# Kernel optimization log

Measured on AMD Instinct MI355X. Metric: run time of the kernel, lower is better.

The kernel has to match this reference:

```python
import jax, jax.numpy as jnp
import numpy as np
from jax.scipy.special import logsumexp

# config constants (match init_kwargs)
EPS_SH, IT_SH = 0.05, 10      # shared-space sinkhorn
EPS_AN, IT_AN = 0.05, 10      # anchor-space sinkhorn
TEMP_SAIL, BIAS_SAIL = 10.0, 0.0
CLAMP = 1e-8


def _rownorm(x):
    return x / jnp.clip(jnp.linalg.norm(x, axis=1, keepdims=True), CLAMP)


def cosine_similarity_matrix(a, b):
    return _rownorm(a) @ _rownorm(b).T


def sinkhorn(dist, epsilon, max_iter):
    """Log-domain Sinkhorn with uniform marginals. dist: (nx, ny)."""
    nx, ny = dist.shape
    M = -dist / epsilon                      # (nx, ny) log kernel
    log_a = -jnp.log(jnp.float32(nx))
    log_b = -jnp.log(jnp.float32(ny))

    def step(carry, _):
        u, v = carry
        u = log_a - logsumexp(M + v[None, :], axis=1)
        v = log_b - logsumexp(M + u[:, None], axis=0)
        return (u, v), None

    init = (jnp.zeros((nx,), M.dtype), jnp.zeros((ny,), M.dtype))
    (u, v), _ = jax.lax.scan(step, init, None, length=max_iter)
    log_plan = M + u[:, None] + v[None, :]
    return jnp.exp(log_plan), log_plan


def setup_inputs() -> dict:
    key = jax.random.key(0)
    ks = jax.random.split(key, 8)
    return {
        "fX_pairs": jax.random.normal(ks[0], (2048, 256), jnp.float32),
        "fY_pairs": jax.random.normal(ks[1], (2048, 256), jnp.float32),
        "X":        jax.random.normal(ks[2], (4096, 768), jnp.float32),
        "Y":        jax.random.normal(ks[3], (4096, 512), jnp.float32),
        "fX":       jax.random.normal(ks[4], (4096, 256), jnp.float32),
        "fY":       jax.random.normal(ks[5], (4096, 256), jnp.float32),
        "X_anchor": jax.random.normal(ks[6], (4096, 768), jnp.float32),
        "Y_anchor": jax.random.normal(ks[7], (4096, 512), jnp.float32),
    }


def _forward(fX_pairs, fY_pairs, X, Y, fX, fY, X_anchor, Y_anchor):
    # --- anchor covariances ---
    Xa, Ya = _rownorm(X_anchor), _rownorm(Y_anchor)
    Na = jnp.float32(Xa.shape[0])
    Sxx = (Xa.T @ Xa) / Na
    Syy = (Ya.T @ Ya) / Na
    Sxy = (Xa.T @ Ya) / Na

    # --- latent-space transport plans (shared sinkhorn) ---
    plan_p, logp_p = sinkhorn(-cosine_similarity_matrix(fX_pairs, fY_pairs), EPS_SH, IT_SH)
    plan_u, logp_u = sinkhorn(-cosine_similarity_matrix(fX, fY), EPS_SH, IT_SH)

    # --- marginal loss: marginals should be uniform ---
    def marginal_loss(plan):
        nx, ny = plan.shape
        a = jnp.full((nx,), 1.0 / nx, plan.dtype)
        b = jnp.full((ny,), 1.0 / ny, plan.dtype)
        return ((plan.sum(1) - a) ** 2).sum() + ((plan.sum(0) - b) ** 2).sum()

    L_marg = marginal_loss(plan_p) + marginal_loss(plan_u)

    # --- SAIL sigmoid contrastive loss on pairs ---
    N = fX_pairs.shape[0]
    cos = cosine_similarity_matrix(fX_pairs, fY_pairs)
    target = -1.0 + 2.0 * jnp.eye(N, dtype=cos.dtype)
    L_sail = -jnp.mean(jax.nn.log_sigmoid(cos * TEMP_SAIL * target - BIAS_SAIL))

    # --- supervised explicit: cosine distance on pairs ---
    L_exp = jnp.mean((1.0 - (_rownorm(fX_pairs) * _rownorm(fY_pairs)).sum(-1)) / 2.0)

    # --- supervised implicit: diag of log plan vs uniform identity ---
    L_imp = -jnp.mean(jnp.diag(logp_p) + jnp.log(jnp.float32(N)))

    # --- anchor-space plan (torch.no_grad -> stop_gradient) ---
    nX = jnp.clip(jnp.sqrt((X * (X @ Sxx)).sum(-1, keepdims=True)), CLAMP)
    nY = jnp.clip(jnp.sqrt((Y * (Y @ Syy)).sum(-1, keepdims=True)), CLAMP)
    Xn, Yn = X / nX, Y / nY
    plan_a, logp_a = jax.lax.stop_gradient(sinkhorn(-(Xn @ Sxy @ Yn.T), EPS_AN, IT_AN))
    Xn = jax.lax.stop_gradient(Xn)
    Yn = jax.lax.stop_gradient(Yn)

    # --- semisupervised OT: KL(plan_anchor || plan_latent) ---
    L_ot = (plan_a * (logp_a - logp_u)).sum()

    # --- semisupervised divergence (frobenius) ---
    fXn, fYn = _rownorm(fX), _rownorm(fY)
    norm1 = (((Xn.T @ Xn) @ Sxy @ (Yn.T @ Yn)) * Sxy).sum()
    norm2 = ((fXn.T @ fXn) * (fYn.T @ fYn)).sum()
    dot = (((Xn.T @ fXn) @ (fYn.T @ Yn)) * Sxy).sum()
    cste = jnp.float32(X.shape[0] * Y.shape[0])
    L_div = (norm1 + norm2 - 2.0 * dot) / cste

    # --- unsupervised Gromov-Wasserstein-style loss ---
    Xu = jax.lax.stop_gradient(_rownorm(X))
    Yu = jax.lax.stop_gradient(_rownorm(Y))
    Kx = Xu @ Xu.T   # (Nx, Nx)
    Ky = Yu @ Yu.T   # (Ny, Ny)
    a = plan_u.sum(1)
    b = plan_u.sum(0)
    L_gw = (a @ (Kx ** 2) @ a + b @ (Ky ** 2) @ b
            - 2.0 * ((Kx @ plan_u @ Ky) * plan_u).sum())

    return L_marg + L_sail + L_exp + L_imp + L_ot + L_div + L_gw


def reference(fX_pairs, fY_pairs, X, Y, fX, fY, X_anchor, Y_anchor):
    return _forward(fX_pairs, fY_pairs, X, Y, fX, fY, X_anchor, Y_anchor)
```

## Files before the change

kernel.cpp:

```cpp
#include <hip/hip_runtime.h>
#include <hip/hip_bf16.h>
#include <math.h>

using u16 = unsigned short;
using s8v = __attribute__((ext_vector_type(8))) short;
using s4v = __attribute__((ext_vector_type(4))) short;
using f4v = __attribute__((ext_vector_type(4))) float;

__device__ __forceinline__ float b2f(u16 x) {
    unsigned int u = ((unsigned int)x) << 16;
    return __uint_as_float(u);
}
__device__ __forceinline__ u16 f2b(float f) {
    unsigned int x = __float_as_uint(f);
    unsigned int r = x + 0x7fffu + ((x >> 16) & 1u);
    return (u16)(r >> 16);
}

__device__ __forceinline__ void a16(u16* lds, const u16* g) {
    __builtin_amdgcn_global_load_lds((__attribute__((address_space(1))) void*)g,
                                     (__attribute__((address_space(3))) void*)lds,
                                     16, 0, 0);
}

__device__ __forceinline__ float block_sum(float v, float* buf) {
    int t = threadIdx.x;
    buf[t] = v; __syncthreads();
    for (int s = 128; s > 0; s >>= 1) {
        if (t < s) buf[t] += buf[t + s];
        __syncthreads();
    }
    float r = buf[0];
    __syncthreads();
    return r;
}

__device__ __forceinline__ float wave_sum(float v) {
#pragma unroll
    for (int off = 32; off; off >>= 1) v += __shfl_xor(v, off, 64);
    return v;
}

__device__ __forceinline__ void block_atomic4(float wval, float* slot) {
    __shared__ float wb[4];
    int lane = threadIdx.x & 63, wv = threadIdx.x >> 6;
    if (lane == 0) wb[wv] = wval;
    __syncthreads();
    if (threadIdx.x == 0) atomicAdd(slot, wb[0] + wb[1] + wb[2] + wb[3]);
}

#define TBM 128
#define TBN 128
#define TBK 32

template<int EPI>
__global__ __launch_bounds__(256)
void gemm_bt(const u16* __restrict__ A, const u16* __restrict__ B,
             float* __restrict__ Cf, u16* __restrict__ Cb,
             int M, int N, int K, int ld, float alpha)
{
    __shared__ __align__(16) u16 As[TBM * TBK];
    __shared__ __align__(16) u16 Bs[TBN * TBK];

    const int tid  = threadIdx.x;
    const int lane = tid & 63;
    const int wave = tid >> 6;
    const int wm   = (wave >> 1) * 64;
    const int wn   = (wave & 1) * 64;
    const int l16  = lane & 15;
    const int q4   = lane >> 4;
    const size_t row0 = (size_t)blockIdx.y * TBM;
    const size_t col0 = (size_t)blockIdx.x * TBN;
    const int kOff = blockIdx.z * K;

    f4v acc[4][4];
#pragma unroll
    for (int mt = 0; mt < 4; ++mt)
#pragma unroll
        for (int nt = 0; nt < 4; ++nt)
#pragma unroll
            for (int r = 0; r < 4; ++r)
                acc[mt][nt][r] = 0.f;

    const int ar0 = wave * 32 + (lane >> 2);
    const int ar1 = ar0 + 16;
    const int akk = (lane & 3) * 8;
    const u16* gA0 = A + (row0 + ar0) * ld + kOff + akk;
    const u16* gA1 = A + (row0 + ar1) * ld + kOff + akk;
    const u16* gB0 = B + (col0 + ar0) * ld + kOff + akk;
    const u16* gB1 = B + (col0 + ar1) * ld + kOff + akk;
    u16* lA0 = As + wave * 1024;
    u16* lA1 = As + wave * 1024 + 512;
    u16* lB0 = Bs + wave * 1024;
    u16* lB1 = Bs + wave * 1024 + 512;

    for (int k0 = 0; k0 < K; k0 += TBK) {
        __syncthreads();
        a16(lA0, gA0 + k0);
        a16(lA1, gA1 + k0);
        a16(lB0, gB0 + k0);
        a16(lB1, gB1 + k0);
        __syncthreads();

        s8v af[4], bfr[4];
#pragma unroll
        for (int mt = 0; mt < 4; ++mt)
            af[mt] = *(const s8v*)(As + (wm + mt * 16 + l16) * TBK + q4 * 8);
#pragma unroll
        for (int nt = 0; nt < 4; ++nt)
            bfr[nt] = *(const s8v*)(Bs + (wn + nt * 16 + l16) * TBK + q4 * 8);
#pragma unroll
        for (int mt = 0; mt < 4; ++mt)
#pragma unroll
            for (int nt = 0; nt < 4; ++nt)
                acc[mt][nt] = __builtin_amdgcn_mfma_f32_16x16x32_bf16(af[mt], bfr[nt], acc[mt][nt], 0, 0, 0);
    }

#pragma unroll
    for (int mt = 0; mt < 4; ++mt)
#pragma unroll
        for (int nt = 0; nt < 4; ++nt)
#pragma unroll
            for (int r = 0; r < 4; ++r) {
                size_t row = row0 + wm + mt * 16 + q4 * 4 + r;
                size_t col = col0 + wn + nt * 16 + l16;
                float v = acc[mt][nt][r] * alpha;
                if (EPI == 0)      Cf[row * (size_t)N + col] = v;
                else if (EPI == 1) Cb[row * (size_t)N + col] = f2b(v);
                else               atomicAdd(&Cf[row * (size_t)N + col], v);
            }
}

struct BG { const u16* A; const u16* B; float* C; int M, Nn, tN, tEnd; };
struct BGArgs { BG d[6]; int n; float alpha; };

__global__ __launch_bounds__(256)
void bgemm(BGArgs g)
{
    __shared__ __align__(16) u16 As[TBM * TBK];
    __shared__ __align__(16) u16 Bs[TBN * TBK];

    int bi = 0;
    while (bi < g.n - 1 && (int)blockIdx.x >= g.d[bi].tEnd) ++bi;
    const BG& d = g.d[bi];
    const int tStart = bi ? g.d[bi - 1].tEnd : 0;
    const int local = blockIdx.x - tStart;
    const int tm = local / d.tN;
    const int tn = local - tm * d.tN;

    const int tid  = threadIdx.x;
    const int lane = tid & 63;
    const int wave = tid >> 6;
    const int wm   = (wave >> 1) * 64;
    const int wn   = (wave & 1) * 64;
    const int l16  = lane & 15;
    const int q4   = lane >> 4;
    const size_t row0 = (size_t)tm * TBM;
    const size_t col0 = (size_t)tn * TBN;
    const int kOff = blockIdx.y * 512;
    const int ld = 4096;

    f4v acc[4][4];
#pragma unroll
    for (int mt = 0; mt < 4; ++mt)
#pragma unroll
        for (int nt = 0; nt < 4; ++nt)
#pragma unroll
            for (int r = 0; r < 4; ++r)
                acc[mt][nt][r] = 0.f;

    const int ar0 = wave * 32 + (lane >> 2);
    const int ar1 = ar0 + 16;
    const int akk = (lane & 3) * 8;
    const u16* gA0 = d.A + (row0 + ar0) * ld + kOff + akk;
    const u16* gA1 = d.A + (row0 + ar1) * ld + kOff + akk;
    const u16* gB0 = d.B + (col0 + ar0) * ld + kOff + akk;
    const u16* gB1 = d.B + (col0 + ar1) * ld + kOff + akk;
    u16* lA0 = As + wave * 1024;
    u16* lA1 = As + wave * 1024 + 512;
    u16* lB0 = Bs + wave * 1024;
    u16* lB1 = Bs + wave * 1024 + 512;

    for (int k0 = 0; k0 < 512; k0 += TBK) {
        __syncthreads();
        a16(lA0, gA0 + k0);
        a16(lA1, gA1 + k0);
        a16(lB0, gB0 + k0);
        a16(lB1, gB1 + k0);
        __syncthreads();

        s8v af[4], bfr[4];
#pragma unroll
        for (int mt = 0; mt < 4; ++mt)
            af[mt] = *(const s8v*)(As + (wm + mt * 16 + l16) * TBK + q4 * 8);
#pragma unroll
        for (int nt = 0; nt < 4; ++nt)
            bfr[nt] = *(const s8v*)(Bs + (wn + nt * 16 + l16) * TBK + q4 * 8);
#pragma unroll
        for (int mt = 0; mt < 4; ++mt)
#pragma unroll
            for (int nt = 0; nt < 4; ++nt)
                acc[mt][nt] = __builtin_amdgcn_mfma_f32_16x16x32_bf16(af[mt], bfr[nt], acc[mt][nt], 0, 0, 0);
    }

#pragma unroll
    for (int mt = 0; mt < 4; ++mt)
#pragma unroll
        for (int nt = 0; nt < 4; ++nt)
#pragma unroll
            for (int r = 0; r < 4; ++r) {
                size_t row = row0 + wm + mt * 16 + q4 * 4 + r;
                size_t col = col0 + wn + nt * 16 + l16;
                atomicAdd(&d.C[row * (size_t)d.Nn + col], acc[mt][nt][r] * g.alpha);
            }
}

struct RN { const float* in; u16* out; int C; int rEnd; };
struct RNArgs { RN d[8]; int n; };

__global__ __launch_bounds__(256)
void rownorm_batch(RNArgs a) {
    int gw = (blockIdx.x * 256 + threadIdx.x) >> 6;
    int lane = threadIdx.x & 63;
    int i = 0;
    while (i < a.n - 1 && gw >= a.d[i].rEnd) ++i;
    if (gw >= a.d[i].rEnd) return;
    int row = gw - (i ? a.d[i - 1].rEnd : 0);
    int C = a.d[i].C;
    const float4* r4 = (const float4*)(a.d[i].in + (size_t)row * C);
    int nv = C >> 2;
    float ss = 0.f;
    for (int c = lane; c < nv; c += 64) {
        float4 v = r4[c];
        ss += v.x * v.x + v.y * v.y + v.z * v.z + v.w * v.w;
    }
    ss = wave_sum(ss);
    float inv = 1.f / fmaxf(sqrtf(ss), 1e-8f);
    s4v* o4 = (s4v*)(a.d[i].out + (size_t)row * C);
    for (int c = lane; c < nv; c += 64) {
        float4 v = r4[c];
        s4v o;
        o[0] = (short)f2b(v.x * inv); o[1] = (short)f2b(v.y * inv);
        o[2] = (short)f2b(v.z * inv); o[3] = (short)f2b(v.w * inv);
        o4[c] = o;
    }
}

__global__ __launch_bounds__(256)
void mahal_w(const u16* __restrict__ Xh, const float* __restrict__ XS,
             u16* __restrict__ out, int nrows, int C) {
    int row = (blockIdx.x * 256 + threadIdx.x) >> 6;
    int lane = threadIdx.x & 63;
    if (row >= nrows) return;
    const s4v* x4 = (const s4v*)(Xh + (size_t)row * C);
    const float4* s4 = (const float4*)(XS + (size_t)row * C);
    int nv = C >> 2;
    float s = 0.f;
    for (int c = lane; c < nv; c += 64) {
        s4v x = x4[c]; float4 v = s4[c];
        s += b2f((u16)x[0]) * v.x + b2f((u16)x[1]) * v.y
           + b2f((u16)x[2]) * v.z + b2f((u16)x[3]) * v.w;
    }
    s = wave_sum(s);
    float inv = 1.f / fmaxf(sqrtf(fmaxf(s, 0.f)), 1e-8f);
    s4v* o4 = (s4v*)(out + (size_t)row * C);
    for (int c = lane; c < nv; c += 64) {
        s4v x = x4[c], o;
#pragma unroll
        for (int k = 0; k < 4; ++k) o[k] = (short)f2b(b2f((u16)x[k]) * inv);
        o4[c] = o;
    }
}

struct TP { const u16* in; u16* out; int R, C, tC, tEnd; const float* s; };
struct TPArgs { TP d[6]; int n; };

__global__ __launch_bounds__(256)
void transpose_batch(TPArgs a) {
    __shared__ u16 tile[32][33];
    int t = blockIdx.x;
    int i = 0;
    while (i < a.n - 1 && t >= a.d[i].tEnd) ++i;
    int local = t - (i ? a.d[i - 1].tEnd : 0);
    const TP& d = a.d[i];
    int ty = local / d.tC, tx = local - ty * d.tC;
    int bx = tx * 32, by = ty * 32;
    int lx = threadIdx.x & 31;
    int lyy = threadIdx.x >> 5;
    for (int r = lyy; r < 32; r += 8)
        tile[r][lx] = d.in[(size_t)(by + r) * d.C + bx + lx];
    __syncthreads();
    for (int r = lyy; r < 32; r += 8) {
        u16 val = tile[lx][r];
        if (d.s) val = f2b(b2f(val) * d.s[by + lx]);
        d.out[(size_t)(bx + r) * d.R + by + lx] = val;
    }
}

__global__ __launch_bounds__(256)
void cast_f2b(const float* __restrict__ in, u16* __restrict__ out, int n) {
    for (int i = blockIdx.x * 256 + threadIdx.x; i < n; i += gridDim.x * 256)
        out[i] = f2b(in[i]);
}

__device__ __forceinline__ float row_sumexp(const u16* __restrict__ rowp,
                                            const float* __restrict__ vin,
                                            int ny, float scale, int lane) {
    const s8v* r8 = (const s8v*)rowp;
    const float4* v4 = (const float4*)vin;
    int nv = ny >> 3;
    float s = 0.f;
    for (int c = lane; c < nv; c += 64) {
        s8v v8 = r8[c];
        float4 va = v4[c * 2], vb = v4[c * 2 + 1];
        s += __expf(b2f((u16)v8[0]) * scale + va.x);
        s += __expf(b2f((u16)v8[1]) * scale + va.y);
        s += __expf(b2f((u16)v8[2]) * scale + va.z);
        s += __expf(b2f((u16)v8[3]) * scale + va.w);
        s += __expf(b2f((u16)v8[4]) * scale + vb.x);
        s += __expf(b2f((u16)v8[5]) * scale + vb.y);
        s += __expf(b2f((u16)v8[6]) * scale + vb.z);
        s += __expf(b2f((u16)v8[7]) * scale + vb.w);
    }
    return wave_sum(s);
}

__global__ __launch_bounds__(256)
void row_lse_tri(const u16* __restrict__ C1, const float* __restrict__ v1, float* __restrict__ u1,
                 const u16* __restrict__ C2, const float* __restrict__ v2, float* __restrict__ u2,
                 const u16* __restrict__ C3, const float* __restrict__ v3, float* __restrict__ u3,
                 float scale, float lm12, float lm3) {
    int gw = (blockIdx.x * 256 + threadIdx.x) >> 6;
    int lane = threadIdx.x & 63;
    if (gw < 4096) {
        float s = row_sumexp(C1 + (size_t)gw * 4096, v1, 4096, scale, lane);
        if (lane == 0) u1[gw] = lm12 - __logf(s);
    } else if (gw < 8192) {
        int row = gw - 4096;
        float s = row_sumexp(C2 + (size_t)row * 4096, v2, 4096, scale, lane);
        if (lane == 0) u2[row] = lm12 - __logf(s);
    } else {
        int row = gw - 8192;
        if (row >= 2048) return;
        float s = row_sumexp(C3 + (size_t)row * 2048, v3, 2048, scale, lane);
        if (lane == 0) u3[row] = lm3 - __logf(s);
    }
}

__device__ __forceinline__ float plan_body(const u16* __restrict__ rowp, u16* __restrict__ prow,
                                           float ui, const float* __restrict__ vin,
                                           int ny, float scale, int lane) {
    const s8v* r8 = (const s8v*)rowp;
    s8v* p8 = (s8v*)prow;
    const float4* v4 = (const float4*)vin;
    int nv = ny >> 3;
    float s = 0.f;
    for (int c = lane; c < nv; c += 64) {
        s8v v8 = r8[c], pb;
        float4 va = v4[c * 2], vb = v4[c * 2 + 1];
        float vv[8] = {va.x, va.y, va.z, va.w, vb.x, vb.y, vb.z, vb.w};
#pragma unroll
        for (int k = 0; k < 8; ++k) {
            float p = __expf(b2f((u16)v8[k]) * scale + ui + vv[k]);
            s += p;
            pb[k] = (short)f2b(p);
        }
        if (p8) p8[c] = pb;
    }
    return wave_sum(s);
}

__global__ __launch_bounds__(256)
void plan_quad(const u16* __restrict__ Cu, const u16* __restrict__ CuT,
               const u16* __restrict__ cosp, const u16* __restrict__ cospT,
               const float* __restrict__ uu, const float* __restrict__ vu,
               const float* __restrict__ up, const float* __restrict__ vp,
               u16* __restrict__ plan,
               float* __restrict__ au, float* __restrict__ bu,
               float* __restrict__ ap, float* __restrict__ bp, float scale) {
    int gw = (blockIdx.x * 256 + threadIdx.x) >> 6;
    int lane = threadIdx.x & 63;
    if (gw < 4096) {
        float s = plan_body(Cu + (size_t)gw * 4096, plan + (size_t)gw * 4096, uu[gw], vu, 4096, scale, lane);
        if (lane == 0) au[gw] = s;
    } else if (gw < 8192) {
        int r = gw - 4096;
        float s = plan_body(CuT + (size_t)r * 4096, nullptr, vu[r], uu, 4096, scale, lane);
        if (lane == 0) bu[r] = s;
    } else if (gw < 10240) {
        int r = gw - 8192;
        float s = plan_body(cosp + (size_t)r * 2048, nullptr, up[r], vp, 2048, scale, lane);
        if (lane == 0) ap[r] = s;
    } else {
        int r = gw - 10240;
        if (r >= 2048) return;
        float s = plan_body(cospT + (size_t)r * 2048, nullptr, vp[r], up, 2048, scale, lane);
        if (lane == 0) bp[r] = s;
    }
}

__global__ __launch_bounds__(256)
void marg4(const float* __restrict__ ap, const float* __restrict__ bp,
           const float* __restrict__ au, const float* __restrict__ bu,
           float* __restrict__ slot) {
    const float* sv; int n; float target;
    if (blockIdx.x == 0)      { sv = ap; n = 2048; target = 1.f / 2048.f; }
    else if (blockIdx.x == 1) { sv = bp; n = 2048; target = 1.f / 2048.f; }
    else if (blockIdx.x == 2) { sv = au; n = 4096; target = 1.f / 4096.f; }
    else                      { sv = bu; n = 4096; target = 1.f / 4096.f; }
    int t = threadIdx.x;
    float s = 0.f;
    for (int i = t; i < n; i += 256) { float d = sv[i] - target; s += d * d; }
    __shared__ float buf[256];
    float tot = block_sum(s, buf);
    if (t == 0) atomicAdd(slot, tot);
}

__global__ __launch_bounds__(256)
void ot_row_w(const u16* __restrict__ Ca, const u16* __restrict__ Cu,
              const float* __restrict__ ua, const float* __restrict__ va,
              const float* __restrict__ uu, const float* __restrict__ vu,
              int nrows, int ny, float scale, float* __restrict__ slot) {
    int row = (blockIdx.x * 256 + threadIdx.x) >> 6;
    int lane = threadIdx.x & 63;
    float local = 0.f;
    if (row < nrows) {
        const s8v* ra = (const s8v*)(Ca + (size_t)row * ny);
        const s8v* ru = (const s8v*)(Cu + (size_t)row * ny);
        const float4* va4 = (const float4*)va;
        const float4* vu4 = (const float4*)vu;
        float uai = ua[row], uui = uu[row];
        int nv = ny >> 3;
        for (int c = lane; c < nv; c += 64) {
            s8v a8 = ra[c], u8 = ru[c];
            float4 a0 = va4[c * 2], a1 = va4[c * 2 + 1];
            float4 u0 = vu4[c * 2], u1 = vu4[c * 2 + 1];
            float av[8] = {a0.x, a0.y, a0.z, a0.w, a1.x, a1.y, a1.z, a1.w};
            float uv[8] = {u0.x, u0.y, u0.z, u0.w, u1.x, u1.y, u1.z, u1.w};
#pragma unroll
            for (int k = 0; k < 8; ++k) {
                float lpa = b2f((u16)a8[k]) * scale + uai + av[k];
                float lpu = b2f((u16)u8[k]) * scale + uui + uv[k];
                local += __expf(lpa) * (lpa - lpu);
            }
        }
    }
    local = wave_sum(local);
    block_atomic4(local, slot);
}

__global__ __launch_bounds__(256)
void sail_row_w(const u16* __restrict__ cosb, int n, float temp, float* __restrict__ slot) {
    int row = (blockIdx.x * 256 + threadIdx.x) >> 6;
    int lane = threadIdx.x & 63;
    float local = 0.f;
    if (row < n) {
        const s8v* r8 = (const s8v*)(cosb + (size_t)row * n);
        int nv = n >> 3;
        for (int c = lane; c < nv; c += 64) {
            s8v v8 = r8[c];
#pragma unroll
            for (int k = 0; k < 8; ++k) {
                int j = c * 8 + k;
                float cv = b2f((u16)v8[k]);
                float wgt = cv * ((j == row) ? temp : -temp);
                local -= fminf(wgt, 0.f) - log1pf(__expf(-fabsf(wgt)));
            }
        }
    }
    local = wave_sum(local);
    block_atomic4(local, slot);
}

__global__ __launch_bounds__(256)
void diag2(const u16* __restrict__ cosb, const float* __restrict__ up,
           const float* __restrict__ vp, int n, float scale,
           float* __restrict__ slotExp, float* __restrict__ slotImp) {
    int t = threadIdx.x;
    float e = 0.f, im = 0.f;
    float logn = logf((float)n);
    for (int i = t; i < n; i += 256) {
        float c = b2f(cosb[(size_t)i * n + i]);
        e  += (1.f - c) * 0.5f;
        im += scale * c + up[i] + vp[i] + logn;
    }
    __shared__ float buf[256];
    float te = block_sum(e, buf);
    float ti = block_sum(im, buf);
    if (t == 0) { atomicAdd(slotExp, te); atomicAdd(slotImp, ti); }
}

__global__ __launch_bounds__(256)
void dotT(const float* __restrict__ Mf, const u16* __restrict__ Tb, int R, int Cc,
          float* __restrict__ slot) {
    int t = threadIdx.x;
    int total = R * Cc;
    float local = 0.f;
    for (int idx = blockIdx.x * 256 + t; idx < total; idx += gridDim.x * 256) {
        int a = idx / Cc, b = idx - a * Cc;
        local += Mf[idx] * b2f(Tb[(size_t)b * R + a]);
    }
    __shared__ float buf[256];
    float tot = block_sum(local, buf);
    if (t == 0) atomicAdd(slot, tot);
}

__global__ __launch_bounds__(256)
void dot_bb(const u16* __restrict__ A, const u16* __restrict__ B, int n,
            float* __restrict__ slot) {
    int t = threadIdx.x;
    float local = 0.f;
    for (int i = blockIdx.x * 256 + t; i < n; i += gridDim.x * 256)
        local += b2f(A[i]) * b2f(B[i]);
    __shared__ float buf[256];
    float tot = block_sum(local, buf);
    if (t == 0) atomicAdd(slot, tot);
}

__global__ __launch_bounds__(256)
void dot3(const float* __restrict__ A, const float* __restrict__ B, const float* __restrict__ C,
          int na, int nb, int nc, float* __restrict__ sA, float* __restrict__ sB, float* __restrict__ sC) {
    const float* p; int n, b0, nblk; float* slot;
    if (blockIdx.x < 32)      { p = A; n = na; b0 = 0;  nblk = 32; slot = sA; }
    else if (blockIdx.x < 48) { p = B; n = nb; b0 = 32; nblk = 16; slot = sB; }
    else                      { p = C; n = nc; b0 = 48; nblk = 16; slot = sC; }
    int t = threadIdx.x;
    float local = 0.f;
    for (int i = (blockIdx.x - b0) * 256 + t; i < n; i += nblk * 256) {
        float v = p[i]; local += v * v;
    }
    __shared__ float buf[256];
    float tot = block_sum(local, buf);
    if (t == 0) atomicAdd(slot, tot);
}

__global__ void combine(const float* __restrict__ s, float* __restrict__ out) {
    if (threadIdx.x == 0 && blockIdx.x == 0) {
        float Np = 2048.f;
        float Nu2 = 4096.f * 4096.f;
        float total = s[0]
                    + s[1] / (Np * Np)
                    + s[2] / Np
                    - s[3] / Np
                    + s[4]
                    + (s[5] + s[6] - 2.f * s[7]) / Nu2
                    + s[8] + s[9] - 2.f * s[10];
        out[0] = total;
    }
}

extern "C" void kernel_launch(void* const* d_in, const int* in_sizes, int n_in,
                              void* d_out, int out_size, void* d_ws, size_t ws_size,
                              hipStream_t stream) {
    const float* fXp_in = (const float*)d_in[0];
    const float* fYp_in = (const float*)d_in[1];
    const float* X_in   = (const float*)d_in[2];
    const float* Y_in   = (const float*)d_in[3];
    const float* fX_in  = (const float*)d_in[4];
    const float* fY_in  = (const float*)d_in[5];
    const float* Xa_in  = (const float*)d_in[6];
    const float* Ya_in  = (const float*)d_in[7];
    float* out = (float*)d_out;

    char* w = (char*)d_ws;
    size_t off = 0;
    auto alloc = [&](size_t bytes) -> char* {
        char* p = w + off;
        off += (bytes + 255) & ~(size_t)255;
        return p;
    };

    const size_t N = 4096, Np = 2048, DX = 768, DY = 512, DF = 256;

    const size_t SLOT = N * N * 2;
    char* S1 = alloc(SLOT);
    char* S2 = alloc(SLOT);
    char* S3 = alloc(SLOT);
    char* S4 = alloc(SLOT);
    char* S5 = alloc(SLOT);

    u16* Xa   = (u16*)S1;
    u16* Cu   = (u16*)S1;
    u16* T1T  = (u16*)S1;
    u16* Ya   = (u16*)S2;
    u16* CuT  = (u16*)S2;
    u16* XuT  = (u16*)S2;
    u16* YuT  = (u16*)(S2 + N * DX * 2);
    u16* Ca   = (u16*)S3;
    u16* XsT  = (u16*)S3;
    u16* YsT  = (u16*)(S3 + N * DX * 2);
    u16* XaT  = (u16*)S4;
    u16* YaT  = (u16*)(S4 + N * DX * 2);
    float* XS = (float*)S4;
    u16* XnT  = (u16*)S4;
    u16* YnT  = (u16*)(S4 + N * DX * 2);
    u16* CaT  = (u16*)S4;
    float* YS = (float*)S5;
    u16* Tb   = (u16*)S5;
    u16* plan = (u16*)S5;

    u16* fXp  = (u16*)alloc(Np * DF * 2);
    u16* fYp  = (u16*)alloc(Np * DF * 2);
    u16* fXn  = (u16*)alloc(N * DF * 2);
    u16* fYn  = (u16*)alloc(N * DF * 2);
    u16* fXnT = (u16*)alloc(N * DF * 2);
    u16* fYnT = (u16*)alloc(N * DF * 2);
    u16* Xu   = (u16*)alloc(N * DX * 2);
    u16* Yu   = (u16*)alloc(N * DY * 2);
    u16* Xn   = (u16*)alloc(N * DX * 2);
    u16* Yn   = (u16*)alloc(N * DY * 2);
    u16* Sxx  = (u16*)alloc(DX * DX * 2);
    u16* Syy  = (u16*)alloc(DY * DY * 2);
    u16* SxyT = (u16*)alloc(DY * DX * 2);
    u16* Gx   = (u16*)alloc(DX * DX * 2);
    u16* Gy   = (u16*)alloc(DY * DY * 2);
    u16* Gfx  = (u16*)alloc(DF * DF * 2);
    u16* Gfy  = (u16*)alloc(DF * DF * 2);
    u16* A1b  = (u16*)alloc(DX * DF * 2);
    u16* B1Tb = (u16*)alloc(DY * DF * 2);
    u16* Hb   = (u16*)alloc(DX * DY * 2);
    u16* cosp = (u16*)alloc(Np * Np * 2);
    u16* cospT= (u16*)alloc(Np * Np * 2);
    float* ap = (float*)alloc(Np * 4);
    float* bp = (float*)alloc(Np * 4);
    float* au = (float*)alloc(N * 4);
    float* bu = (float*)alloc(N * 4);

    char* zero_begin = w + off;
    float* slots = (float*)alloc(64 * 4);
    float* up = (float*)alloc(Np * 4);
    float* vp = (float*)alloc(Np * 4);
    float* uu = (float*)alloc(N * 4);
    float* vu = (float*)alloc(N * 4);
    float* ua = (float*)alloc(N * 4);
    float* va = (float*)alloc(N * 4);
    float* SxxF  = (float*)alloc(DX * DX * 4);
    float* SyyF  = (float*)alloc(DY * DY * 4);
    float* SxyTF = (float*)alloc(DY * DX * 4);
    float* GxF   = (float*)alloc(DX * DX * 4);
    float* GyF   = (float*)alloc(DY * DY * 4);
    float* GfxF  = (float*)alloc(DF * DF * 4);
    float* GfyF  = (float*)alloc(DF * DF * 4);
    float* A1F   = (float*)alloc(DX * DF * 4);
    float* B1F   = (float*)alloc(DY * DF * 4);
    float* HbF   = (float*)alloc(DX * DY * 4);
    float* H2    = (float*)alloc(DX * DY * 4);
    float* D1    = (float*)alloc(DX * DY * 4);
    float* W1F   = (float*)alloc(DX * DX * 4);
    float* W2F   = (float*)alloc(DY * DY * 4);
    float* MF    = (float*)alloc(DX * DY * 4);
    size_t zero_bytes = (size_t)((w + off) - zero_begin);

    const float SCALE = 20.f;

#define GEMM_F32(A_, B_, C_, M_, N_, K_, al_) \
    gemm_bt<0><<<dim3((N_) / 128, (M_) / 128), 256, 0, stream>>>((A_), (B_), (C_), nullptr, (M_), (N_), (K_), (K_), (al_))
#define GEMM_B16(A_, B_, C_, M_, N_, K_, al_) \
    gemm_bt<1><<<dim3((N_) / 128, (M_) / 128), 256, 0, stream>>>((A_), (B_), nullptr, (C_), (M_), (N_), (K_), (K_), (al_))
#define GEMM_SKF(A_, B_, CF_, M_, N_, Kfull_, SPL_, al_) \
    gemm_bt<3><<<dim3((N_) / 128, (M_) / 128, (SPL_)), 256, 0, stream>>>((A_), (B_), (CF_), nullptr, (M_), (N_), (Kfull_) / (SPL_), (Kfull_), (al_))

    hipMemsetAsync(zero_begin, 0, zero_bytes, stream);

    {
        RNArgs a;
        a.d[0] = {Xa_in, Xa, 768, 4096};
        a.d[1] = {Ya_in, Ya, 512, 8192};
        a.d[2] = {fXp_in, fXp, 256, 10240};
        a.d[3] = {fYp_in, fYp, 256, 12288};
        a.d[4] = {fX_in, fXn, 256, 16384};
        a.d[5] = {fY_in, fYn, 256, 20480};
        a.d[6] = {X_in, Xu, 768, 24576};
        a.d[7] = {Y_in, Yu, 512, 28672};
        a.n = 8;
        rownorm_batch<<<7168, 256, 0, stream>>>(a);
    }

    {
        TPArgs a;
        a.d[0] = {Xa, XaT, 4096, 768, 24, 3072, nullptr};
        a.d[1] = {Ya, YaT, 4096, 512, 16, 5120, nullptr};
        a.d[2] = {fXn, fXnT, 4096, 256, 8, 6144, nullptr};
        a.d[3] = {fYn, fYnT, 4096, 256, 8, 7168, nullptr};
        a.n = 4;
        transpose_batch<<<7168, 256, 0, stream>>>(a);
    }

    {
        BGArgs g;
        g.d[0] = {XaT, XaT, SxxF, 768, 768, 6, 36};
        g.d[1] = {YaT, YaT, SyyF, 512, 512, 4, 52};
        g.d[2] = {YaT, XaT, SxyTF, 512, 768, 6, 76};
        g.n = 3; g.alpha = 1.f / 4096.f;
        bgemm<<<dim3(76, 8), 256, 0, stream>>>(g);
        cast_f2b<<<256, 256, 0, stream>>>(SxxF, Sxx, 768 * 768 + 512 * 512 + 512 * 768);
    }

    GEMM_F32(Xu, Sxx, XS, 4096, 768, 768, 1.f);
    GEMM_F32(Yu, Syy, YS, 4096, 512, 512, 1.f);
    mahal_w<<<1024, 256, 0, stream>>>(Xu, XS, Xn, 4096, 768);
    mahal_w<<<1024, 256, 0, stream>>>(Yu, YS, Yn, 4096, 512);

    {
        TPArgs a;
        a.d[0] = {Xn, XnT, 4096, 768, 24, 3072, nullptr};
        a.d[1] = {Yn, YnT, 4096, 512, 16, 5120, nullptr};
        a.n = 2;
        transpose_batch<<<5120, 256, 0, stream>>>(a);
    }

    {
        BGArgs g;
        g.d[0] = {XnT, XnT, GxF, 768, 768, 6, 36};
        g.d[1] = {YnT, YnT, GyF, 512, 512, 4, 52};
        g.d[2] = {fXnT, fXnT, GfxF, 256, 256, 2, 56};
        g.d[3] = {fYnT, fYnT, GfyF, 256, 256, 2, 60};
        g.d[4] = {XnT, fXnT, A1F, 768, 256, 2, 72};
        g.d[5] = {YnT, fYnT, B1F, 512, 256, 2, 80};
        g.n = 6; g.alpha = 1.f;
        bgemm<<<dim3(80, 8), 256, 0, stream>>>(g);
        cast_f2b<<<256, 256, 0, stream>>>(GxF, Gx,
            768 * 768 + 512 * 512 + 256 * 256 + 256 * 256 + 768 * 256 + 512 * 256);
    }

    GEMM_B16(fXp, fYp, cosp, 2048, 2048, 256, 1.f);
    GEMM_B16(fYp, fXp, cospT, 2048, 2048, 256, 1.f);

    GEMM_SKF(Gx, SxyT, HbF, 768, 512, 768, 4, 1.f);
    cast_f2b<<<256, 256, 0, stream>>>(HbF, Hb, 768 * 512);
    GEMM_SKF(Hb, Gy, H2, 768, 512, 512, 4, 1.f);
    GEMM_SKF(A1b, B1Tb, D1, 768, 512, 256, 2, 1.f);
    dotT<<<192, 256, 0, stream>>>(H2, SxyT, 768, 512, slots + 5);
    dot_bb<<<64, 256, 0, stream>>>(Gfx, Gfy, 256 * 256, slots + 6);
    dotT<<<192, 256, 0, stream>>>(D1, SxyT, 768, 512, slots + 7);

    GEMM_B16(Xn, SxyT, Tb, 4096, 512, 768, 1.f);
    GEMM_B16(Tb, Yn, Ca, 4096, 4096, 512, 1.f);
    GEMM_B16(Yn, Tb, CaT, 4096, 4096, 512, 1.f);
    GEMM_B16(fXn, fYn, Cu, 4096, 4096, 256, 1.f);
    GEMM_B16(fYn, fXn, CuT, 4096, 4096, 256, 1.f);

    {
        float lm12 = -logf(4096.f), lm3 = -logf(2048.f);
        for (int it = 0; it < 10; ++it) {
            row_lse_tri<<<2560, 256, 0, stream>>>(Cu, vu, uu, Ca, va, ua, cosp, vp, up, SCALE, lm12, lm3);
            row_lse_tri<<<2560, 256, 0, stream>>>(CuT, uu, vu, CaT, ua, va, cospT, up, vp, SCALE, lm12, lm3);
        }
    }

    plan_quad<<<3072, 256, 0, stream>>>(Cu, CuT, cosp, cospT, uu, vu, up, vp,
                                        plan, au, bu, ap, bp, SCALE);
    marg4<<<4, 256, 0, stream>>>(ap, bp, au, bu, slots + 0);
    diag2<<<1, 256, 0, stream>>>(cosp, up, vp, 2048, SCALE, slots + 2, slots + 3);
    sail_row_w<<<512, 256, 0, stream>>>(cosp, 2048, 10.f, slots + 1);

    ot_row_w<<<1024, 256, 0, stream>>>(Ca, Cu, ua, va, uu, vu, 4096, 4096, SCALE, slots + 4);

    {
        TPArgs a;
        a.d[0] = {Xu, XuT, 4096, 768, 24, 3072, nullptr};
        a.d[1] = {Yu, YuT, 4096, 512, 16, 5120, nullptr};
        a.d[2] = {Xu, XsT, 4096, 768, 24, 8192, au};
        a.d[3] = {Yu, YsT, 4096, 512, 16, 10240, bu};
        a.n = 4;
        transpose_batch<<<10240, 256, 0, stream>>>(a);
    }
    GEMM_B16(YuT, plan, T1T, 512, 4096, 4096, 1.f);
    {
        BGArgs g;
        g.d[0] = {XsT, XuT, W1F, 768, 768, 6, 36};
        g.d[1] = {YsT, YuT, W2F, 512, 512, 4, 52};
        g.n = 2; g.alpha = 1.f;
        bgemm<<<dim3(52, 8), 256, 0, stream>>>(g);
    }
    {
        BGArgs g;
        g.d[0] = {XuT, T1T, MF, 768, 512, 4, 24};
        g.n = 1; g.alpha = 1.f;
        bgemm<<<dim3(24, 8), 256, 0, stream>>>(g);
    }
    dot3<<<64, 256, 0, stream>>>(W1F, W2F, MF, 768 * 768, 512 * 512, 768 * 512,
                                 slots + 8, slots + 9, slots + 10);

    combine<<<1, 1, 0, stream>>>(slots, out);

#undef GEMM_F32
#undef GEMM_B16
#undef GEMM_SKF
}
```

Before: 986.1 us.

## Generalize batched GEMM, fuse dot epilogues, transpose instead of recomputing transposed GEMMs

Replaces the fixed-shape batched GEMM with a templated version that has configurable K chunk, leading dimension and epilogue. It uses this to batch several independent GEMMs into single launches, and to fold the H2/D1 Frobenius dot products into the GEMM epilogue so the dotT kernels and their intermediate buffers go away. The transposed similarity matrices (CuT, cospT, CaT) now come from a batched transpose instead of separate GEMMs. The T1T GEMM becomes a split-K atomic GEMM batched with W1/W2, followed by a cast. This cuts launches and redundant GEMM work, at the cost of extra atomics, a memset and a cast pass.

```diff
diff --git a/kernel.cpp b/kernel.cpp
--- a/kernel.cpp
+++ b/kernel.cpp
@@ -125,24 +125,29 @@
                 size_t row = row0 + wm + mt * 16 + q4 * 4 + r;
                 size_t col = col0 + wn + nt * 16 + l16;
                 float v = acc[mt][nt][r] * alpha;
-                if (EPI == 0)      Cf[row * (size_t)N + col] = v;
-                else if (EPI == 1) Cb[row * (size_t)N + col] = f2b(v);
-                else               atomicAdd(&Cf[row * (size_t)N + col], v);
+                if (EPI == 1) Cb[row * (size_t)N + col] = f2b(v);
+                else          atomicAdd(&Cf[row * (size_t)N + col], v);
             }
 }
 
-struct BG { const u16* A; const u16* B; float* C; int M, Nn, tN, tEnd; };
-struct BGArgs { BG d[6]; int n; float alpha; };
-
-__global__ __launch_bounds__(256)
-void bgemm(BGArgs g)
+struct BGN {
+    const u16* A; const u16* B;
+    float* Cf; u16* Cb;
+    const u16* W; float* slot;
+    int M, N, Kc, ld, WL, tN, tEnd;
+};
+struct BGNArgs { BGN d[6]; int n; float alpha; };
+
+template<int EPI>
+__global__ __launch_bounds__(256)
+void bgemmN(BGNArgs g)
 {
     __shared__ __align__(16) u16 As[TBM * TBK];
     __shared__ __align__(16) u16 Bs[TBN * TBK];
 
     int bi = 0;
     while (bi < g.n - 1 && (int)blockIdx.x >= g.d[bi].tEnd) ++bi;
-    const BG& d = g.d[bi];
+    const BGN& d = g.d[bi];
     const int tStart = bi ? g.d[bi - 1].tEnd : 0;
     const int local = blockIdx.x - tStart;
     const int tm = local / d.tN;
@@ -157,8 +162,8 @@
     const int q4   = lane >> 4;
     const size_t row0 = (size_t)tm * TBM;
     const size_t col0 = (size_t)tn * TBN;
-    const int kOff = blockIdx.y * 512;
-    const int ld = 4096;
+    const int kOff = blockIdx.y * d.Kc;
+    const int ld = d.ld;
 
     f4v acc[4][4];
 #pragma unroll
@@ -181,7 +186,7 @@
     u16* lB0 = Bs + wave * 1024;
     u16* lB1 = Bs + wave * 1024 + 512;
 
-    for (int k0 = 0; k0 < 512; k0 += TBK) {
+    for (int k0 = 0; k0 < d.Kc; k0 += TBK) {
         __syncthreads();
         a16(lA0, gA0 + k0);
         a16(lA1, gA1 + k0);
@@ -203,16 +208,36 @@
                 acc[mt][nt] = __builtin_amdgcn_mfma_f32_16x16x32_bf16(af[mt], bfr[nt], acc[mt][nt], 0, 0, 0);
     }
 
-#pragma unroll
-    for (int mt = 0; mt < 4; ++mt)
-#pragma unroll
-        for (int nt = 0; nt < 4; ++nt)
-#pragma unroll
-            for (int r = 0; r < 4; ++r) {
-                size_t row = row0 + wm + mt * 16 + q4 * 4 + r;
-                size_t col = col0 + wn + nt * 16 + l16;
-                atomicAdd(&d.C[row * (size_t)d.Nn + col], acc[mt][nt][r] * g.alpha);
-            }
+    if (EPI == 2) {
+        float local2 = 0.f;
+#pragma unroll
+        for (int mt = 0; mt < 4; ++mt)
+#pragma unroll
+            for (int nt = 0; nt < 4; ++nt)
+#pragma unroll
+                for (int r = 0; r < 4; ++r) {
+                    size_t row = row0 + wm + mt * 16 + q4 * 4 + r;
+                    size_t col = col0 + wn + nt * 16 + l16;
+                    local2 += acc[mt][nt][r] * b2f(d.W[col * (size_t)d.WL + row]);
+                }
+        __shared__ float red[256];
+        float tot = block_sum(local2 * g.alpha, red);
+        if (tid == 0) atomicAdd(d.slot, tot);
+    } else {
+#pragma unroll
+        for (int mt = 0; mt < 4; ++mt)
+#pragma unroll
+            for (int nt = 0; nt < 4; ++nt)
+#pragma unroll
+                for (int r = 0; r < 4; ++r) {
+                    size_t row = row0 + wm + mt * 16 + q4 * 4 + r;
+                    size_t col = col0 + wn + nt * 16 + l16;
+                    float v = acc[mt][nt][r] * g.alpha;
+                    if (EPI == 0)      d.Cf[row * (size_t)d.N + col] = v;
+                    else if (EPI == 1) d.Cb[row * (size_t)d.N + col] = f2b(v);
+                    else               atomicAdd(&d.Cf[row * (size_t)d.N + col], v);
+                }
+    }
 }
 
 struct RN { const float* in; u16* out; int C; int rEnd; };
@@ -491,21 +516,6 @@
 }
 
 __global__ __launch_bounds__(256)
-void dotT(const float* __restrict__ Mf, const u16* __restrict__ Tb, int R, int Cc,
-          float* __restrict__ slot) {
-    int t = threadIdx.x;
-    int total = R * Cc;
-    float local = 0.f;
-    for (int idx = blockIdx.x * 256 + t; idx < total; idx += gridDim.x * 256) {
-        int a = idx / Cc, b = idx - a * Cc;
-        local += Mf[idx] * b2f(Tb[(size_t)b * R + a]);
-    }
-    __shared__ float buf[256];
-    float tot = block_sum(local, buf);
-    if (t == 0) atomicAdd(slot, tot);
-}
-
-__global__ __launch_bounds__(256)
 void dot_bb(const u16* __restrict__ A, const u16* __restrict__ B, int n,
             float* __restrict__ slot) {
     int t = threadIdx.x;
@@ -595,6 +605,7 @@
     u16* XnT  = (u16*)S4;
     u16* YnT  = (u16*)(S4 + N * DX * 2);
     u16* CaT  = (u16*)S4;
+    float* T1F= (float*)S4;
     float* YS = (float*)S5;
     u16* Tb   = (u16*)S5;
     u16* plan = (u16*)S5;
@@ -644,21 +655,12 @@
     float* A1F   = (float*)alloc(DX * DF * 4);
     float* B1F   = (float*)alloc(DY * DF * 4);
     float* HbF   = (float*)alloc(DX * DY * 4);
-    float* H2    = (float*)alloc(DX * DY * 4);
-    float* D1    = (float*)alloc(DX * DY * 4);
     float* W1F   = (float*)alloc(DX * DX * 4);
     float* W2F   = (float*)alloc(DY * DY * 4);
     float* MF    = (float*)alloc(DX * DY * 4);
     size_t zero_bytes = (size_t)((w + off) - zero_begin);
 
     const float SCALE = 20.f;
-
-#define GEMM_F32(A_, B_, C_, M_, N_, K_, al_) \
-    gemm_bt<0><<<dim3((N_) / 128, (M_) / 128), 256, 0, stream>>>((A_), (B_), (C_), nullptr, (M_), (N_), (K_), (K_), (al_))
-#define GEMM_B16(A_, B_, C_, M_, N_, K_, al_) \
-    gemm_bt<1><<<dim3((N_) / 128, (M_) / 128), 256, 0, stream>>>((A_), (B_), nullptr, (C_), (M_), (N_), (K_), (K_), (al_))
-#define GEMM_SKF(A_, B_, CF_, M_, N_, Kfull_, SPL_, al_) \
-    gemm_bt<3><<<dim3((N_) / 128, (M_) / 128, (SPL_)), 256, 0, stream>>>((A_), (B_), (CF_), nullptr, (M_), (N_), (Kfull_) / (SPL_), (Kfull_), (al_))
 
     hipMemsetAsync(zero_begin, 0, zero_bytes, stream);
 
@@ -687,17 +689,22 @@
     }
 
     {
-        BGArgs g;
-        g.d[0] = {XaT, XaT, SxxF, 768, 768, 6, 36};
-        g.d[1] = {YaT, YaT, SyyF, 512, 512, 4, 52};
-        g.d[2] = {YaT, XaT, SxyTF, 512, 768, 6, 76};
+        BGNArgs g;
+        g.d[0] = {XaT, XaT, SxxF, nullptr, nullptr, nullptr, 768, 768, 512, 4096, 0, 6, 36};
+        g.d[1] = {YaT, YaT, SyyF, nullptr, nullptr, nullptr, 512, 512, 512, 4096, 0, 4, 52};
+        g.d[2] = {YaT, XaT, SxyTF, nullptr, nullptr, nullptr, 512, 768, 512, 4096, 0, 6, 76};
         g.n = 3; g.alpha = 1.f / 4096.f;
-        bgemm<<<dim3(76, 8), 256, 0, stream>>>(g);
+        bgemmN<3><<<dim3(76, 8), 256, 0, stream>>>(g);
         cast_f2b<<<256, 256, 0, stream>>>(SxxF, Sxx, 768 * 768 + 512 * 512 + 512 * 768);
     }
 
-    GEMM_F32(Xu, Sxx, XS, 4096, 768, 768, 1.f);
-    GEMM_F32(Yu, Syy, YS, 4096, 512, 512, 1.f);
+    {
+        BGNArgs g;
+        g.d[0] = {Xu, Sxx, XS, nullptr, nullptr, nullptr, 4096, 768, 768, 768, 0, 6, 192};
+        g.d[1] = {Yu, Syy, YS, nullptr, nullptr, nullptr, 4096, 512, 512, 512, 0, 4, 320};
+        g.n = 2; g.alpha = 1.f;
+        bgemmN<0><<<dim3(320, 1), 256, 0, stream>>>(g);
+    }
     mahal_w<<<1024, 256, 0, stream>>>(Xu, XS, Xn, 4096, 768);
     mahal_w<<<1024, 256, 0, stream>>>(Yu, YS, Yn, 4096, 512);
 
@@ -710,35 +717,48 @@
     }
 
     {
-        BGArgs g;
-        g.d[0] = {XnT, XnT, GxF, 768, 768, 6, 36};
-        g.d[1] = {YnT, YnT, GyF, 512, 512, 4, 52};
-        g.d[2] = {fXnT, fXnT, GfxF, 256, 256, 2, 56};
-        g.d[3] = {fYnT, fYnT, GfyF, 256, 256, 2, 60};
-        g.d[4] = {XnT, fXnT, A1F, 768, 256, 2, 72};
-        g.d[5] = {YnT, fYnT, B1F, 512, 256, 2, 80};
+        BGNArgs g;
+        g.d[0] = {XnT, XnT, GxF, nullptr, nullptr, nullptr, 768, 768, 512, 4096, 0, 6, 36};
+        g.d[1] = {YnT, YnT, GyF, nullptr, nullptr, nullptr, 512, 512, 512, 4096, 0, 4, 52};
+        g.d[2] = {fXnT, fXnT, GfxF, nullptr, nullptr, nullptr, 256, 256, 512, 4096, 0, 2, 56};
+        g.d[3] = {fYnT, fYnT, GfyF, nullptr, nullptr, nullptr, 256, 256, 512, 4096, 0, 2, 60};
+        g.d[4] = {XnT, fXnT, A1F, nullptr, nullptr, nullptr, 768, 256, 512, 4096, 0, 2, 72};
+        g.d[5] = {YnT, fYnT, B1F, nullptr, nullptr, nullptr, 512, 256, 512, 4096, 0, 2, 80};
         g.n = 6; g.alpha = 1.f;
-        bgemm<<<dim3(80, 8), 256, 0, stream>>>(g);
+        bgemmN<3><<<dim3(80, 8), 256, 0, stream>>>(g);
         cast_f2b<<<256, 256, 0, stream>>>(GxF, Gx,
             768 * 768 + 512 * 512 + 256 * 256 + 256 * 256 + 768 * 256 + 512 * 256);
     }
 
-    GEMM_B16(fXp, fYp, cosp, 2048, 2048, 256, 1.f);
-    GEMM_B16(fYp, fXp, cospT, 2048, 2048, 256, 1.f);
-
-    GEMM_SKF(Gx, SxyT, HbF, 768, 512, 768, 4, 1.f);
+    {
+        BGNArgs g;
+        g.d[0] = {fXn, fYn, nullptr, Cu, nullptr, nullptr, 4096, 4096, 256, 256, 0, 32, 1024};
+        g.d[1] = {fXp, fYp, nullptr, cosp, nullptr, nullptr, 2048, 2048, 256, 256, 0, 16, 1280};
+        g.d[2] = {Xn, SxyT, nullptr, Tb, nullptr, nullptr, 4096, 512, 768, 768, 0, 4, 1408};
+        g.n = 3; g.alpha = 1.f;
+        bgemmN<1><<<dim3(1408, 1), 256, 0, stream>>>(g);
+    }
+    gemm_bt<1><<<dim3(32, 32), 256, 0, stream>>>(Tb, Yn, nullptr, Ca, 4096, 4096, 512, 512, 1.f);
+
+    {
+        TPArgs a;
+        a.d[0] = {Cu, CuT, 4096, 4096, 128, 16384, nullptr};
+        a.d[1] = {cosp, cospT, 2048, 2048, 64, 20480, nullptr};
+        a.d[2] = {Ca, CaT, 4096, 4096, 128, 36864, nullptr};
+        a.n = 3;
+        transpose_batch<<<36864, 256, 0, stream>>>(a);
+    }
+
+    gemm_bt<3><<<dim3(4, 6, 4), 256, 0, stream>>>(Gx, SxyT, HbF, nullptr, 768, 512, 192, 768, 1.f);
     cast_f2b<<<256, 256, 0, stream>>>(HbF, Hb, 768 * 512);
-    GEMM_SKF(Hb, Gy, H2, 768, 512, 512, 4, 1.f);
-    GEMM_SKF(A1b, B1Tb, D1, 768, 512, 256, 2, 1.f);
-    dotT<<<192, 256, 0, stream>>>(H2, SxyT, 768, 512, slots + 5);
+    {
+        BGNArgs g;
+        g.d[0] = {Hb, Gy, nullptr, nullptr, SxyT, slots + 5, 768, 512, 128, 512, 768, 4, 24};
+        g.d[1] = {A1b, B1Tb, nullptr, nullptr, SxyT, slots + 7, 768, 512, 64, 256, 768, 4, 48};
+        g.n = 2; g.alpha = 1.f;
+        bgemmN<2><<<dim3(48, 4), 256, 0, stream>>>(g);
+    }
     dot_bb<<<64, 256, 0, stream>>>(Gfx, Gfy, 256 * 256, slots + 6);
-    dotT<<<192, 256, 0, stream>>>(D1, SxyT, 768, 512, slots + 7);
-
-    GEMM_B16(Xn, SxyT, Tb, 4096, 512, 768, 1.f);
-    GEMM_B16(Tb, Yn, Ca, 4096, 4096, 512, 1.f);
-    GEMM_B16(Yn, Tb, CaT, 4096, 4096, 512, 1.f);
-    GEMM_B16(fXn, fYn, Cu, 4096, 4096, 256, 1.f);
-    GEMM_B16(fYn, fXn, CuT, 4096, 4096, 256, 1.f);
 
     {
         float lm12 = -logf(4096.f), lm3 = -logf(2048.f);
@@ -765,26 +785,24 @@
         a.n = 4;
         transpose_batch<<<10240, 256, 0, stream>>>(a);
     }
-    GEMM_B16(YuT, plan, T1T, 512, 4096, 4096, 1.f);
-    {
-        BGArgs g;
-        g.d[0] = {XsT, XuT, W1F, 768, 768, 6, 36};
-        g.d[1] = {YsT, YuT, W2F, 512, 512, 4, 52};
-        g.n = 2; g.alpha = 1.f;
-        bgemm<<<dim3(52, 8), 256, 0, stream>>>(g);
-    }
-    {
-        BGArgs g;
-        g.d[0] = {XuT, T1T, MF, 768, 512, 4, 24};
+    hipMemsetAsync(T1F, 0, 512 * 4096 * 4, stream);
+    {
+        BGNArgs g;
+        g.d[0] = {YuT, plan, T1F, nullptr, nullptr, nullptr, 512, 4096, 512, 4096, 0, 32, 128};
+        g.d[1] = {XsT, XuT, W1F, nullptr, nullptr, nullptr, 768, 768, 512, 4096, 0, 6, 164};
+        g.d[2] = {YsT, YuT, W2F, nullptr, nullptr, nullptr, 512, 512, 512, 4096, 0, 4, 180};
+        g.n = 3; g.alpha = 1.f;
+        bgemmN<3><<<dim3(180, 8), 256, 0, stream>>>(g);
+    }
+    cast_f2b<<<512, 256, 0, stream>>>(T1F, T1T, 512 * 4096);
+    {
+        BGNArgs g;
+        g.d[0] = {XuT, T1T, MF, nullptr, nullptr, nullptr, 768, 512, 512, 4096, 0, 4, 24};
         g.n = 1; g.alpha = 1.f;
-        bgemm<<<dim3(24, 8), 256, 0, stream>>>(g);
+        bgemmN<3><<<dim3(24, 8), 256, 0, stream>>>(g);
     }
     dot3<<<64, 256, 0, stream>>>(W1F, W2F, MF, 768 * 768, 512 * 512, 768 * 512,
                                  slots + 8, slots + 9, slots + 10);
 
     combine<<<1, 1, 0, stream>>>(slots, out);
-
-#undef GEMM_F32
-#undef GEMM_B16
-#undef GEMM_SKF
-}
+}
```

Result: faster. 917.2 us (-7.0%).
